# Kernel optimization log

Measured on AMD Instinct MI355X. Metric: run time of the kernel, lower is better.

## Reference

```python
import jax, jax.numpy as jnp
import numpy as np
from math import sqrt

B, S, Q, L = 16, 1024, 8, 512
D_FEA, D_KEYS, D_MODEL = 128, 128, 128


def setup_inputs() -> dict:
    key = jax.random.key(0)
    ks = jax.random.split(key, 10)
    s = 0.02
    return {
        "target_embedding": jax.random.normal(ks[0], (B, S, D_FEA), dtype=jnp.float32),
        "source_embedding": jax.random.normal(ks[1], (B, Q, L, D_KEYS), dtype=jnp.float32),
        "Wq": jax.random.normal(ks[2], (D_FEA, D_MODEL), dtype=jnp.float32) * s,
        "bq": jnp.zeros((D_MODEL,), dtype=jnp.float32),
        "Wk": jax.random.normal(ks[3], (D_KEYS, D_MODEL), dtype=jnp.float32) * s,
        "bk": jnp.zeros((D_MODEL,), dtype=jnp.float32),
        "Wv": jax.random.normal(ks[4], (D_KEYS, D_MODEL), dtype=jnp.float32) * s,
        "bv": jnp.zeros((D_MODEL,), dtype=jnp.float32),
        "Wo": jax.random.normal(ks[5], (D_MODEL, D_FEA), dtype=jnp.float32) * s,
        "bo": jnp.zeros((D_FEA,), dtype=jnp.float32),
    }


def reference(target_embedding, source_embedding, Wq, bq, Wk, bk, Wv, bv, Wo, bo):
    # Projections
    q = target_embedding @ Wq + bq            # [B,S,E]
    k = source_embedding @ Wk + bk            # [B,Q,L,E]
    v = source_embedding @ Wv + bv            # [B,Q,L,E]
    E = q.shape[-1]
    scale = 1.0 / sqrt(E)
    # Nonstandard 4D scores: [B,Q,S,L]
    scores = jnp.einsum('bse,bqle->bqsl', q, k)
    A = jax.nn.softmax(scale * scores, axis=-1)  # softmax over l; dropout = identity (eval)
    # Weighted sum reduces over BOTH q and l -> [B,S,E]
    out = jnp.einsum('bqsl,bqle->bse', A, v)
    return out @ Wo + bo
```

## Files before the change

### kernel.cpp

```cpp
#include <hip/hip_runtime.h>
#include <hip/hip_bf16.h>

#define TB 16
#define TS 1024
#define TQ 8
#define TL 512
#define TD 128

typedef __attribute__((ext_vector_type(8))) short bf16x8;
typedef __attribute__((ext_vector_type(4))) short short4v;
typedef __attribute__((ext_vector_type(4))) float f32x4;
typedef __attribute__((ext_vector_type(4))) float float4v;

__device__ __forceinline__ short f2bf(float f) {
    union { float fv; unsigned u; } v; v.fv = f;
    unsigned r = v.u + 0x7fffu + ((v.u >> 16) & 1u);
    return (short)(r >> 16);
}
__device__ __forceinline__ float bf2f(short s) {
    union { unsigned u; float f; } v; v.u = ((unsigned)(unsigned short)s) << 16;
    return v.f;
}

#define OFF_Q   0u
#define OFF_K   (4u << 20)
#define OFF_V   (OFF_K + (16u << 20))
#define OFF_P0  (OFF_V + (16u << 20))
#define OFF_W   (OFF_P0 + (4u << 20))

__global__ void prep_w(const float* __restrict__ Wq, const float* __restrict__ Wk,
                       const float* __restrict__ Wv, const float* __restrict__ Wo,
                       short* __restrict__ wt) {
    const float* srcs[4] = {Wq, Wk, Wv, Wo};
    const int m = blockIdx.x >> 3;
    const float* s = srcs[m];
    short* dst = wt + m * (TD * TD);
    const int off = (blockIdx.x & 7) * 2048;
    for (int i = threadIdx.x; i < 2048; i += 256) {
        int idx = off + i;
        int k = idx >> 7, e = idx & 127;
        dst[e * TD + k] = f2bf(s[idx]);
    }
}

__global__ __launch_bounds__(256) void proj_all(const float* __restrict__ target,
                                                const float* __restrict__ source,
                                                const short* __restrict__ wt,
                                                const float* __restrict__ biasq,
                                                const float* __restrict__ biask,
                                                const float* __restrict__ biasv,
                                                short* __restrict__ qb,
                                                short* __restrict__ kb,
                                                short* __restrict__ vf) {
    __shared__ short xt[32][136];
    const int t = threadIdx.x;
    const int lane = t & 63, w = t >> 6;
    const int lane16 = lane & 15, g = lane >> 4;
    const bool iskv = blockIdx.x < 2048;
    const int r0 = (iskv ? blockIdx.x : (blockIdx.x - 2048)) * 32;
    const float* X = iskv ? source : target;

#pragma unroll
    for (int it = 0; it < 4; ++it) {
        int f4 = t + it * 256;
        int row = f4 >> 5, col = (f4 & 31) * 4;
        float4v x = *reinterpret_cast<const float4v*>(&X[(long)(r0 + row) * TD + col]);
        short4v s;
        s[0] = f2bf(x[0]); s[1] = f2bf(x[1]); s[2] = f2bf(x[2]); s[3] = f2bf(x[3]);
        *reinterpret_cast<short4v*>(&xt[row][col]) = s;
    }
    __syncthreads();

    const int n0 = w * 32;
    bf16x8 a[2][4];
#pragma unroll
    for (int mi = 0; mi < 2; ++mi)
#pragma unroll
        for (int kt = 0; kt < 4; ++kt)
            a[mi][kt] = *reinterpret_cast<const bf16x8*>(&xt[mi * 16 + lane16][kt * 32 + g * 8]);

    const f32x4 Z = {0.f, 0.f, 0.f, 0.f};
    if (iskv) {
        const short* Wtk = wt + 1 * TD * TD;
        const short* Wtv = wt + 2 * TD * TD;
        f32x4 ak[2][2] = {{Z, Z}, {Z, Z}};
        f32x4 av[2][2] = {{Z, Z}, {Z, Z}};
#pragma unroll
        for (int ni = 0; ni < 2; ++ni)
#pragma unroll
            for (int kt = 0; kt < 4; ++kt) {
                bf16x8 bkf = *reinterpret_cast<const bf16x8*>(
                    &Wtk[(n0 + ni * 16 + lane16) * TD + kt * 32 + g * 8]);
                bf16x8 bvf = *reinterpret_cast<const bf16x8*>(
                    &Wtv[(n0 + ni * 16 + lane16) * TD + kt * 32 + g * 8]);
#pragma unroll
                for (int mi = 0; mi < 2; ++mi) {
                    ak[mi][ni] = __builtin_amdgcn_mfma_f32_16x16x32_bf16(bkf, a[mi][kt], ak[mi][ni], 0, 0, 0);
                    av[mi][ni] = __builtin_amdgcn_mfma_f32_16x16x32_bf16(a[mi][kt], bvf, av[mi][ni], 0, 0, 0);
                }
            }
#pragma unroll
        for (int mi = 0; mi < 2; ++mi)
#pragma unroll
            for (int ni = 0; ni < 2; ++ni) {
                int e0 = n0 + ni * 16 + g * 4;
                float4v kb4 = *reinterpret_cast<const float4v*>(&biask[e0]);
                int row = r0 + mi * 16 + lane16;
                short4v ks;
#pragma unroll
                for (int reg = 0; reg < 4; ++reg) ks[reg] = f2bf(ak[mi][ni][reg] + kb4[reg]);
                *reinterpret_cast<short4v*>(&kb[(long)row * TD + e0]) = ks;
                int e = n0 + ni * 16 + lane16;
                float bbv = biasv[e];
                int row0 = r0 + mi * 16 + g * 4;
                int bq = row0 >> 9;
                int l = row0 & 511;
                int k32 = l >> 5, j8 = (l >> 3) & 3, jb = l & 7;
                long off = (long)bq * (TL * TD) +
                           ((((long)(k32 * 8 + (e >> 4)) * 4 + j8) * 16) + (e & 15)) * 8 + jb;
                short4v sv;
#pragma unroll
                for (int reg = 0; reg < 4; ++reg) sv[reg] = f2bf(av[mi][ni][reg] + bbv);
                *reinterpret_cast<short4v*>(&vf[off]) = sv;
            }
    } else {
        const short* Wtq = wt;
        const float CS = 0.08838834764831845f * 1.4426950408889634f;
        f32x4 aq[2][2] = {{Z, Z}, {Z, Z}};
#pragma unroll
        for (int ni = 0; ni < 2; ++ni)
#pragma unroll
            for (int kt = 0; kt < 4; ++kt) {
                bf16x8 bqf = *reinterpret_cast<const bf16x8*>(
                    &Wtq[(n0 + ni * 16 + lane16) * TD + kt * 32 + g * 8]);
#pragma unroll
                for (int mi = 0; mi < 2; ++mi)
                    aq[mi][ni] = __builtin_amdgcn_mfma_f32_16x16x32_bf16(bqf, a[mi][kt], aq[mi][ni], 0, 0, 0);
            }
#pragma unroll
        for (int mi = 0; mi < 2; ++mi)
#pragma unroll
            for (int ni = 0; ni < 2; ++ni) {
                int e0 = n0 + ni * 16 + g * 4;
                float4v qb4 = *reinterpret_cast<const float4v*>(&biasq[e0]);
                int row = r0 + mi * 16 + lane16;
                short4v qs;
#pragma unroll
                for (int reg = 0; reg < 4; ++reg) qs[reg] = f2bf((aq[mi][ni][reg] + qb4[reg]) * CS);
                *reinterpret_cast<short4v*>(&qb[(long)row * TD + e0]) = qs;
            }
    }
}

__global__ __launch_bounds__(256, 2) void attn_k(const short* __restrict__ qb,
                                                 const short* __restrict__ kb,
                                                 const short* __restrict__ vf,
                                                 short* __restrict__ po0,
                                                 float* __restrict__ po1) {
    __shared__ float cmb[2][4][2][16];
    __shared__ float red[2][2][8][4][16][4];
    const int t = threadIdx.x;
    const int lane = t & 63, w = t >> 6;
    const int lane16 = lane & 15, g = lane >> 4;

    int idx = blockIdx.x;
    int xcd = idx & 7, slot = idx >> 3;
    const int b = xcd * 2 + (slot >> 6);
    const int rem = slot & 63;
    const int qh = rem >> 5;
    const int s0 = (rem & 31) * 32;

    bf16x8 qf[2][4];
#pragma unroll
    for (int sg = 0; sg < 2; ++sg) {
        const short* qrow = qb + (long)(b * TS + s0 + sg * 16 + lane16) * TD;
#pragma unroll
        for (int kt = 0; kt < 4; ++kt)
            qf[sg][kt] = *reinterpret_cast<const bf16x8*>(qrow + kt * 32 + g * 8);
    }

    const f32x4 Z = {0.f, 0.f, 0.f, 0.f};
    f32x4 o[2][8];
#pragma unroll
    for (int sg = 0; sg < 2; ++sg)
#pragma unroll
        for (int et = 0; et < 8; ++et) o[sg][et] = Z;

    const int arow = 8 * (lane16 >> 2) + (lane16 & 3);

    for (int qi = qh * 4; qi < qh * 4 + 4; ++qi) {
        const long kvb = (long)(b * TQ + qi) * (TL * TD);
        const short* Kw = kb + kvb + (long)(w * 128) * TD;

        f32x4 sacc[2][8];
#pragma unroll
        for (int sg = 0; sg < 2; ++sg)
#pragma unroll
            for (int lt = 0; lt < 8; ++lt) sacc[sg][lt] = Z;
#pragma unroll
        for (int lt = 0; lt < 8; ++lt) {
            const short* krow = Kw + (long)(32 * (lt >> 1) + 4 * (lt & 1) + arow) * TD;
            bf16x8 ka[4];
#pragma unroll
            for (int kt = 0; kt < 4; ++kt)
                ka[kt] = *reinterpret_cast<const bf16x8*>(krow + kt * 32 + g * 8);
#pragma unroll
            for (int kt = 0; kt < 4; ++kt) {
                sacc[0][lt] = __builtin_amdgcn_mfma_f32_16x16x32_bf16(ka[kt], qf[0][kt], sacc[0][lt], 0, 0, 0);
                sacc[1][lt] = __builtin_amdgcn_mfma_f32_16x16x32_bf16(ka[kt], qf[1][kt], sacc[1][lt], 0, 0, 0);
            }
        }

#pragma unroll
        for (int sg = 0; sg < 2; ++sg) {
            float sum = 0.f;
#pragma unroll
            for (int lt = 0; lt < 8; ++lt)
#pragma unroll
                for (int r = 0; r < 4; ++r) {
                    float e = exp2f(sacc[sg][lt][r]);
                    sacc[sg][lt][r] = e;
                    sum += e;
                }
            sum += __shfl_xor(sum, 16);
            sum += __shfl_xor(sum, 32);
            if (lane < 16) cmb[qi & 1][w][sg][lane16] = sum;
        }
        __syncthreads();
        float Fs[2];
#pragma unroll
        for (int sg = 0; sg < 2; ++sg)
            Fs[sg] = 1.f / (cmb[qi & 1][0][sg][lane16] + cmb[qi & 1][1][sg][lane16]
                          + cmb[qi & 1][2][sg][lane16] + cmb[qi & 1][3][sg][lane16]);

        bf16x8 pa[2][4];
#pragma unroll
        for (int sg = 0; sg < 2; ++sg)
#pragma unroll
            for (int kt = 0; kt < 4; ++kt) {
                union { unsigned u[4]; bf16x8 v; } pk;
#pragma unroll
                for (int h = 0; h < 2; ++h) {
                    float x0 = sacc[sg][2 * kt + h][0] * Fs[sg];
                    float x1 = sacc[sg][2 * kt + h][1] * Fs[sg];
                    float x2 = sacc[sg][2 * kt + h][2] * Fs[sg];
                    float x3 = sacc[sg][2 * kt + h][3] * Fs[sg];
                    asm("v_cvt_pk_bf16_f32 %0, %1, %2" : "=v"(pk.u[2 * h]) : "v"(x0), "v"(x1));
                    asm("v_cvt_pk_bf16_f32 %0, %1, %2" : "=v"(pk.u[2 * h + 1]) : "v"(x2), "v"(x3));
                }
                pa[sg][kt] = pk.v;
            }

#pragma unroll
        for (int kt = 0; kt < 4; ++kt) {
            const short* vbase = vf + kvb + ((long)(w * 4 + kt) * 4096) + g * 128 + lane16 * 8;
#pragma unroll
            for (int et = 0; et < 8; ++et) {
                bf16x8 vb = *reinterpret_cast<const bf16x8*>(vbase + et * 512);
                o[0][et] = __builtin_amdgcn_mfma_f32_16x16x32_bf16(pa[0][kt], vb, o[0][et], 0, 0, 0);
                o[1][et] = __builtin_amdgcn_mfma_f32_16x16x32_bf16(pa[1][kt], vb, o[1][et], 0, 0, 0);
            }
        }
    }

    if (w >= 2) {
#pragma unroll
        for (int sg = 0; sg < 2; ++sg)
#pragma unroll
            for (int et = 0; et < 8; ++et)
                *reinterpret_cast<f32x4*>(&red[w - 2][sg][et][g][lane16][0]) = o[sg][et];
    }
    __syncthreads();
    if (w < 2) {
#pragma unroll
        for (int sg = 0; sg < 2; ++sg)
#pragma unroll
            for (int et = 0; et < 8; ++et)
                o[sg][et] += *reinterpret_cast<f32x4*>(&red[w][sg][et][g][lane16][0]);
    }
    __syncthreads();
    if (w == 1) {
#pragma unroll
        for (int sg = 0; sg < 2; ++sg)
#pragma unroll
            for (int et = 0; et < 8; ++et)
                *reinterpret_cast<f32x4*>(&red[0][sg][et][g][lane16][0]) = o[sg][et];
    }
    __syncthreads();
    if (w == 0) {
#pragma unroll
        for (int sg = 0; sg < 2; ++sg)
#pragma unroll
            for (int et = 0; et < 8; ++et) {
                o[sg][et] += *reinterpret_cast<f32x4*>(&red[0][sg][et][g][lane16][0]);
#pragma unroll
                for (int reg = 0; reg < 4; ++reg) {
                    int s = s0 + sg * 16 + g * 4 + reg;
                    long addr = (long)(b * TS + s) * TD + et * 16 + lane16;
                    if (qh == 0) po0[addr] = f2bf(o[sg][et][reg]);
                    else         po1[addr] = o[sg][et][reg];
                }
            }
    }
}

__global__ __launch_bounds__(256) void comb_proj(const short* __restrict__ po0,
                                                 const short* __restrict__ Wt,
                                                 const float* __restrict__ bias,
                                                 float* __restrict__ out) {
    const int t = threadIdx.x;
    const int lane = t & 63, w = t >> 6;
    const int lane16 = lane & 15, g = lane >> 4;
    const int r0 = blockIdx.x * 32;
    const int n0 = w * 32;

    bf16x8 a[2][4];
#pragma unroll
    for (int mi = 0; mi < 2; ++mi)
#pragma unroll
        for (int kt = 0; kt < 4; ++kt) {
            long base = (long)(r0 + mi * 16 + lane16) * TD + kt * 32 + g * 8;
            float4v x0 = *reinterpret_cast<const float4v*>(&out[base]);
            float4v x1 = *reinterpret_cast<const float4v*>(&out[base + 4]);
            bf16x8 p0 = *reinterpret_cast<const bf16x8*>(&po0[base]);
            bf16x8 af;
#pragma unroll
            for (int j = 0; j < 4; ++j) af[j] = f2bf(x0[j] + bf2f(p0[j]));
#pragma unroll
            for (int j = 0; j < 4; ++j) af[4 + j] = f2bf(x1[j] + bf2f(p0[4 + j]));
            a[mi][kt] = af;
        }
    __syncthreads();

    const f32x4 Z = {0.f, 0.f, 0.f, 0.f};
    f32x4 acc[2][2] = {{Z, Z}, {Z, Z}};
#pragma unroll
    for (int ni = 0; ni < 2; ++ni)
#pragma unroll
        for (int kt = 0; kt < 4; ++kt) {
            bf16x8 wf = *reinterpret_cast<const bf16x8*>(
                &Wt[(n0 + ni * 16 + lane16) * TD + kt * 32 + g * 8]);
#pragma unroll
            for (int mi = 0; mi < 2; ++mi)
                acc[mi][ni] = __builtin_amdgcn_mfma_f32_16x16x32_bf16(wf, a[mi][kt], acc[mi][ni], 0, 0, 0);
        }

#pragma unroll
    for (int mi = 0; mi < 2; ++mi)
#pragma unroll
        for (int ni = 0; ni < 2; ++ni) {
            int e0 = n0 + ni * 16 + g * 4;
            float4v b4 = *reinterpret_cast<const float4v*>(&bias[e0]);
            int row = r0 + mi * 16 + lane16;
            f32x4 res;
#pragma unroll
            for (int reg = 0; reg < 4; ++reg) res[reg] = acc[mi][ni][reg] + b4[reg];
            *reinterpret_cast<f32x4*>(&out[(long)row * TD + e0]) = res;
        }
}

extern "C" void kernel_launch(void* const* d_in, const int* in_sizes, int n_in,
                              void* d_out, int out_size, void* d_ws, size_t ws_size,
                              hipStream_t stream) {
    (void)in_sizes; (void)n_in; (void)out_size; (void)ws_size;
    const float* target = (const float*)d_in[0];
    const float* source = (const float*)d_in[1];
    const float* Wq = (const float*)d_in[2];
    const float* bq = (const float*)d_in[3];
    const float* Wk = (const float*)d_in[4];
    const float* bk = (const float*)d_in[5];
    const float* Wv = (const float*)d_in[6];
    const float* bv = (const float*)d_in[7];
    const float* Wo = (const float*)d_in[8];
    const float* bo = (const float*)d_in[9];

    char* ws = (char*)d_ws;
    short* qb  = (short*)(ws + OFF_Q);
    short* kb  = (short*)(ws + OFF_K);
    short* vf  = (short*)(ws + OFF_V);
    short* po0 = (short*)(ws + OFF_P0);
    short* wt  = (short*)(ws + OFF_W);
    float* out = (float*)d_out;

    prep_w<<<32, 256, 0, stream>>>(Wq, Wk, Wv, Wo, wt);
    proj_all<<<2560, 256, 0, stream>>>(target, source, wt, bq, bk, bv, qb, kb, vf);
    attn_k<<<1024, 256, 0, stream>>>(qb, kb, vf, po0, out);
    comb_proj<<<512, 256, 0, stream>>>(po0, wt + 3 * TD * TD, bo, out);
}
```

Before: 220.7 us.

## Software-pipeline K and V global loads into register ring buffers

Prefetches K fragments into a 4-deep register ring so the global loads for tile lt+4 are issued while tile lt's MFMAs run, and loads the first K tiles of the next q slice during the PV phase. V fragments are double-buffered so the next kt's loads overlap the current MFMAs. The aim is to hide global memory latency behind matrix math, at the cost of many more live VGPRs, which may lower occupancy or cause spills.

```diff
diff --git a/kernel.cpp b/kernel.cpp
--- a/kernel.cpp
+++ b/kernel.cpp
@@ -187,11 +187,25 @@
         for (int et = 0; et < 8; ++et) o[sg][et] = Z;
 
     const int arow = 8 * (lane16 >> 2) + (lane16 & 3);
-
-    for (int qi = qh * 4; qi < qh * 4 + 4; ++qi) {
+    const int q0 = qh * 4;
+
+    auto kload = [&](int qi, int lt, bf16x8* dst) {
+        const short* krow = kb + (long)(b * TQ + qi) * (TL * TD)
+                          + (long)(w * 128 + 32 * (lt >> 1) + 4 * (lt & 1) + arow) * TD;
+#pragma unroll
+        for (int kt = 0; kt < 4; ++kt)
+            dst[kt] = *reinterpret_cast<const bf16x8*>(krow + kt * 32 + g * 8);
+    };
+
+    bf16x8 ka[4][4];
+    kload(q0, 0, ka[0]);
+    kload(q0, 1, ka[1]);
+
+    for (int qi = q0; qi < q0 + 4; ++qi) {
         const long kvb = (long)(b * TQ + qi) * (TL * TD);
-        const short* Kw = kb + kvb + (long)(w * 128) * TD;
-
+
+        kload(qi, 2, ka[2]);
+        kload(qi, 3, ka[3]);
         f32x4 sacc[2][8];
 #pragma unroll
         for (int sg = 0; sg < 2; ++sg)
@@ -199,16 +213,12 @@
             for (int lt = 0; lt < 8; ++lt) sacc[sg][lt] = Z;
 #pragma unroll
         for (int lt = 0; lt < 8; ++lt) {
-            const short* krow = Kw + (long)(32 * (lt >> 1) + 4 * (lt & 1) + arow) * TD;
-            bf16x8 ka[4];
-#pragma unroll
-            for (int kt = 0; kt < 4; ++kt)
-                ka[kt] = *reinterpret_cast<const bf16x8*>(krow + kt * 32 + g * 8);
 #pragma unroll
             for (int kt = 0; kt < 4; ++kt) {
-                sacc[0][lt] = __builtin_amdgcn_mfma_f32_16x16x32_bf16(ka[kt], qf[0][kt], sacc[0][lt], 0, 0, 0);
-                sacc[1][lt] = __builtin_amdgcn_mfma_f32_16x16x32_bf16(ka[kt], qf[1][kt], sacc[1][lt], 0, 0, 0);
-            }
+                sacc[0][lt] = __builtin_amdgcn_mfma_f32_16x16x32_bf16(ka[lt & 3][kt], qf[0][kt], sacc[0][lt], 0, 0, 0);
+                sacc[1][lt] = __builtin_amdgcn_mfma_f32_16x16x32_bf16(ka[lt & 3][kt], qf[1][kt], sacc[1][lt], 0, 0, 0);
+            }
+            if (lt < 4) kload(qi, lt + 4, ka[lt & 3]);
         }
 
 #pragma unroll
@@ -251,14 +261,28 @@
                 pa[sg][kt] = pk.v;
             }
 
+        bf16x8 vb[2][8];
+        {
+            const short* vbase = vf + kvb + ((long)(w * 4) * 4096) + g * 128 + lane16 * 8;
+#pragma unroll
+            for (int et = 0; et < 8; ++et)
+                vb[0][et] = *reinterpret_cast<const bf16x8*>(vbase + et * 512);
+        }
+        int qn = (qi < q0 + 3) ? qi + 1 : qi;
+        kload(qn, 0, ka[0]);
+        kload(qn, 1, ka[1]);
 #pragma unroll
         for (int kt = 0; kt < 4; ++kt) {
-            const short* vbase = vf + kvb + ((long)(w * 4 + kt) * 4096) + g * 128 + lane16 * 8;
+            if (kt < 3) {
+                const short* vbase = vf + kvb + ((long)(w * 4 + kt + 1) * 4096) + g * 128 + lane16 * 8;
+#pragma unroll
+                for (int et = 0; et < 8; ++et)
+                    vb[(kt + 1) & 1][et] = *reinterpret_cast<const bf16x8*>(vbase + et * 512);
+            }
 #pragma unroll
             for (int et = 0; et < 8; ++et) {
-                bf16x8 vb = *reinterpret_cast<const bf16x8*>(vbase + et * 512);
-                o[0][et] = __builtin_amdgcn_mfma_f32_16x16x32_bf16(pa[0][kt], vb, o[0][et], 0, 0, 0);
-                o[1][et] = __builtin_amdgcn_mfma_f32_16x16x32_bf16(pa[1][kt], vb, o[1][et], 0, 0, 0);
+                o[0][et] = __builtin_amdgcn_mfma_f32_16x16x32_bf16(pa[0][kt], vb[kt & 1][et], o[0][et], 0, 0, 0);
+                o[1][et] = __builtin_amdgcn_mfma_f32_16x16x32_bf16(pa[1][kt], vb[kt & 1][et], o[1][et], 0, 0, 0);
             }
         }
     }
```

Result: no change. 223.6 us (+1.3%).
